# Optimization experiments

Measured on AMD Instinct MI355X. Metric: run time of the kernel, lower is better.

The kernel has to match this reference:

```python
import jax, jax.numpy as jnp
import numpy as np
import math

DIM = 1536
HEADS = 4
DIM_KEY = 64
DIM_VALUE = 64
NUM_REL_POS_FEATURES = 64
SEQ_LEN = 4096  # must match the hard-coded positional buffer seq_len in the torch module
SCALE = DIM_KEY ** -0.5


def positional_embed(seq_len, feature_size):
    # get_positional_embed: central-mask features + sign-antisymmetric copy
    distances = jnp.arange(-seq_len + 1, seq_len)  # (2n-1,)
    nb = feature_size // 2  # one feature fn, 2 components
    pow_rate = math.exp(math.log(seq_len + 1) / nb)
    center_widths = jnp.power(jnp.float32(pow_rate), jnp.arange(1, nb + 1, dtype=jnp.float32)) - 1.0
    emb = (center_widths[None, :] > jnp.abs(distances)[:, None]).astype(jnp.float32)  # (2n-1, nb)
    sign = jnp.sign(distances).astype(jnp.float32)[:, None]
    return jnp.concatenate([emb, sign * emb], axis=-1)  # (2n-1, feature_size)


def setup_inputs() -> dict:
    key = jax.random.key(0)
    ks = jax.random.split(key, 9)
    b, n, dim, h, dk, dv, F = 1, SEQ_LEN, DIM, HEADS, DIM_KEY, DIM_VALUE, NUM_REL_POS_FEATURES
    s = 0.02
    x = jax.random.normal(ks[0], (b, n, dim), dtype=jnp.float32)
    Wq = jax.random.normal(ks[1], (dim, h * dk), dtype=jnp.float32) * s
    Wk = jax.random.normal(ks[2], (dim, h * dk), dtype=jnp.float32) * s
    Wv = jax.random.normal(ks[3], (dim, h * dv), dtype=jnp.float32) * s
    W_rel_k = jax.random.normal(ks[4], (F, h * dk), dtype=jnp.float32) * s
    Wo = jax.random.normal(ks[5], (h * dv, dim), dtype=jnp.float32) * s  # torch inits zeros; random for a meaningful test
    bo = jnp.zeros((dim,), dtype=jnp.float32)
    rel_content_bias = jax.random.normal(ks[6], (1, h, 1, dk), dtype=jnp.float32)
    rel_pos_bias = jax.random.normal(ks[7], (1, h, 1, dk), dtype=jnp.float32)
    return {"x": x, "Wq": Wq, "Wk": Wk, "Wv": Wv, "W_rel_k": W_rel_k, "Wo": Wo, "bo": bo,
            "rel_content_bias": rel_content_bias, "rel_pos_bias": rel_pos_bias}


def reference(x, Wq, Wk, Wv, W_rel_k, Wo, bo, rel_content_bias, rel_pos_bias):
    b, n, _ = x.shape
    h, dk, dv = HEADS, DIM_KEY, DIM_VALUE
    # projections -> (b, h, n, d)
    q = (x @ Wq).reshape(b, n, h, dk).transpose(0, 2, 1, 3) * SCALE
    k = (x @ Wk).reshape(b, n, h, dk).transpose(0, 2, 1, 3)
    v = (x @ Wv).reshape(b, n, h, dv).transpose(0, 2, 1, 3)
    # content logits with content bias
    content_logits = jnp.einsum('bhid,bhjd->bhij', q + rel_content_bias, k)
    # relative-position keys from fixed positional buffer (pos_dropout p=0 -> identity)
    positions = positional_embed(SEQ_LEN, NUM_REL_POS_FEATURES)  # (2n-1, F)
    rel_k = (positions @ W_rel_k).reshape(2 * n - 1, h, dk).transpose(1, 0, 2)  # (h, 2n-1, dk)
    # rel logits then Transformer-XL strided shift: rel_logits[i, j] = r[i, n-1 + j - i]
    r = jnp.einsum('bhid,hjd->bhij', q + rel_pos_bias, rel_k)  # (b, h, n, 2n-1)
    idx = (n - 1) + jnp.arange(n)[None, :] - jnp.arange(n)[:, None]  # (n, n)
    rel_logits = jnp.take_along_axis(r, jnp.broadcast_to(idx[None, None], (b, h, n, n)), axis=-1)
    attn = jax.nn.softmax(content_logits + rel_logits, axis=-1)  # attn_dropout p=0 -> identity
    out = jnp.einsum('bhij,bhjd->bhid', attn, v)
    out = out.transpose(0, 2, 1, 3).reshape(b, n, h * dv)
    return out @ Wo + bo
```

## Files before the change

kernel.cpp:

```cpp
#include <hip/hip_runtime.h>
#include <hip/hip_bf16.h>

#define N_SEQ 4096
#define DIMM  1536
#define NH    4
#define DK    64
#define HD    256
#define QK_SCALE 0.125f
#define WSZ   393216
#define KSPLIT 8

typedef __bf16 bf16x8 __attribute__((ext_vector_type(8)));
typedef unsigned short u16;
typedef u16   u16x8  __attribute__((ext_vector_type(8)));
typedef u16   u16x4  __attribute__((ext_vector_type(4)));
typedef float f32x4  __attribute__((ext_vector_type(4)));
typedef float f32x16 __attribute__((ext_vector_type(16)));
typedef unsigned int u32x4 __attribute__((ext_vector_type(4)));

__device__ inline float b2f(u16 u){
    union { float f; unsigned int i; } v; v.i = ((unsigned int)u) << 16; return v.f;
}
__device__ inline u16 f2b(float f){
    __bf16 h = (__bf16)f;
    return __builtin_bit_cast(u16, h);
}
__device__ inline bf16x8 ldfrag(const u16* p){
    return __builtin_bit_cast(bf16x8, *(const u16x8*)p);
}
__device__ inline f32x16 zero16(){
    f32x16 v;
    #pragma unroll
    for (int i = 0; i < 16; ++i) v[i] = 0.f;
    return v;
}
__device__ inline float pair_sum(unsigned int wd){
    union { unsigned int i; float f; } lo, hi;
    lo.i = wd << 16; hi.i = wd & 0xffff0000u;
    return lo.f + hi.f;
}

__global__ __launch_bounds__(256) void convwt_kernel(const float* __restrict__ Wq,
    const float* __restrict__ Wk, const float* __restrict__ Wv, u16* __restrict__ Wt){
    int idx = (blockIdx.x * 256 + threadIdx.x) * 8;
    int s = idx / WSZ, off = idx % WSZ;
    int n = off / DIMM, k = off % DIMM;
    const float* W = (s == 0) ? Wq : (s == 1 ? Wk : Wv);
    u16x8 o;
    #pragma unroll
    for (int e = 0; e < 8; ++e) o[e] = f2b(W[(size_t)(k + e) * HD + n]);
    *(u16x8*)&Wt[idx] = o;
}

__global__ __launch_bounds__(256) void fmtab_kernel(unsigned char* __restrict__ fmt){
    int d = blockIdx.x * 256 + threadIdx.x;
    float lg = logf((float)(N_SEQ + 1)) * (1.0f / 32.0f);
    float ad = (float)d;
    int fm = 0;
    for (int f = 0; f < 32; ++f){
        float cw = expf(lg * (float)(f + 1)) - 1.0f;
        fm += (cw <= ad) ? 1 : 0;
    }
    fmt[d] = (unsigned char)fm;
}

__global__ __launch_bounds__(256) void wsuf_kernel(const float* __restrict__ Wrel,
    u16* __restrict__ WsP, u16* __restrict__ WsM){
    int t = threadIdx.x;
    int h = t >> 6, d = t & 63;
    float a1 = 0.f, a2 = 0.f;
    for (int fm = 31; fm >= 0; --fm){
        a1 += Wrel[(size_t)fm * HD + h * DK + d];
        a2 += Wrel[(size_t)(32 + fm) * HD + h * DK + d];
        WsP[(h * 32 + fm) * 64 + d] = f2b(a1 + a2);
        WsM[(h * 32 + fm) * 64 + d] = f2b(a1 - a2);
    }
}

__global__ __launch_bounds__(256) void qkv_kernel(const float* __restrict__ X,
    const u16* __restrict__ Wt,
    u16* __restrict__ Q, u16* __restrict__ K, u16* __restrict__ Vt){
    __shared__ __align__(16) u16 xs[64 * 72];
    __shared__ __align__(16) u16 bs[64 * 72];
    int s  = blockIdx.x >> 2;
    int n0 = (blockIdx.x & 3) * 64;
    int m0 = blockIdx.y * 64;
    int t = threadIdx.x;
    int w = t >> 6, lane = t & 63, qd = lane >> 4, l15 = lane & 15;
    int r  = t >> 3;
    int cv = (t & 7) * 8;
    f32x4 acc[4] = {{0,0,0,0},{0,0,0,0},{0,0,0,0},{0,0,0,0}};

    f32x4 xa[2], xb[2];
    u16x8 wv[2];
    auto LOAD = [&](int k0){
        #pragma unroll
        for (int rep = 0; rep < 2; ++rep){
            int rr = rep * 32 + r;
            size_t xi = (size_t)(m0 + rr) * DIMM + k0 + cv;
            xa[rep] = *(const f32x4*)(X + xi);
            xb[rep] = *(const f32x4*)(X + xi + 4);
            wv[rep] = *(const u16x8*)&Wt[(size_t)s * WSZ + (size_t)(n0 + rr) * DIMM + k0 + cv];
        }
    };
    auto STORE = [&](){
        #pragma unroll
        for (int rep = 0; rep < 2; ++rep){
            int rr = rep * 32 + r;
            u16x8 xv;
            #pragma unroll
            for (int e = 0; e < 4; ++e){ xv[e] = f2b(xa[rep][e]); xv[4 + e] = f2b(xb[rep][e]); }
            *(u16x8*)&xs[rr * 72 + cv] = xv;
            *(u16x8*)&bs[rr * 72 + cv] = wv[rep];
        }
    };

    LOAD(0);
    for (int k0 = 0; k0 < DIMM; k0 += 64){
        STORE();
        __syncthreads();
        if (k0 + 64 < DIMM) LOAD(k0 + 64);
        bf16x8 a0 = ldfrag(&xs[(w * 16 + l15) * 72 +  0 + qd * 8]);
        bf16x8 a1 = ldfrag(&xs[(w * 16 + l15) * 72 + 32 + qd * 8]);
        #pragma unroll
        for (int nt = 0; nt < 4; ++nt){
            bf16x8 b0 = ldfrag(&bs[(nt * 16 + l15) * 72 +  0 + qd * 8]);
            bf16x8 b1 = ldfrag(&bs[(nt * 16 + l15) * 72 + 32 + qd * 8]);
            acc[nt] = __builtin_amdgcn_mfma_f32_16x16x32_bf16(a0, b0, acc[nt], 0, 0, 0);
            acc[nt] = __builtin_amdgcn_mfma_f32_16x16x32_bf16(a1, b1, acc[nt], 0, 0, 0);
        }
        __syncthreads();
    }

    int row0 = m0 + w * 16 + qd * 4;
    if (s == 0){
        #pragma unroll
        for (int nt = 0; nt < 4; ++nt){
            int col = n0 + nt * 16 + l15;
            #pragma unroll
            for (int reg = 0; reg < 4; ++reg)
                Q[(size_t)(row0 + reg) * HD + col] = f2b(acc[nt][reg] * QK_SCALE);
        }
    } else if (s == 1){
        #pragma unroll
        for (int nt = 0; nt < 4; ++nt){
            int col = n0 + nt * 16 + l15;
            #pragma unroll
            for (int reg = 0; reg < 4; ++reg)
                K[(size_t)(row0 + reg) * HD + col] = f2b(acc[nt][reg]);
        }
    } else {
        #pragma unroll
        for (int nt = 0; nt < 4; ++nt){
            int col = n0 + nt * 16 + l15;
            u16x4 pv;
            #pragma unroll
            for (int reg = 0; reg < 4; ++reg) pv[reg] = f2b(acc[nt][reg]);
            *(u16x4*)&Vt[(size_t)col * N_SEQ + row0] = pv;
        }
    }
}

__global__ __launch_bounds__(256) void attn_kernel(const u16* __restrict__ Q,
    const u16* __restrict__ Kg, const u16* __restrict__ Vt,
    const u16* __restrict__ WsPg, const u16* __restrict__ WsMg,
    const unsigned char* __restrict__ fmtg,
    const float* __restrict__ CB, const float* __restrict__ PB,
    u16* __restrict__ OpU, float* __restrict__ mpart, float* __restrict__ lpart){
    __shared__ __align__(16) unsigned char smem[39936];
    u16* Ks   = (u16*)(smem);
    u16* Vts  = (u16*)(smem + 9216);
    u16* Qs   = (u16*)(smem);
    u16* relP = (u16*)(smem + 18432);
    u16* relM = (u16*)(smem + 27136);
    unsigned char* fmt = smem + 35840;
    u16* WsPs = (u16*)(smem + 18432);
    u16* WsMs = (u16*)(smem + 23040);

    int i0   = blockIdx.x * 128;
    int h    = blockIdx.y;
    int half = blockIdx.z;
    int bid  = blockIdx.x * NH + h;
    int jbase = half * (N_SEQ / KSPLIT);
    const int NT = (N_SEQ / KSPLIT) / 64;
    int t = threadIdx.x;
    int w = t >> 6, lane = t & 63, l31 = lane & 31, hbit = lane >> 5;
    int h8 = hbit * 8;
    int i_loc = w * 32 + l31;

    int sr = t >> 3, scv = (t & 7) * 8;
    u16x8 kr0, kr1, vr0, vr1;
    auto LOAD = [&](int j0){
        kr0 = *(const u16x8*)&Kg[(size_t)(j0 + sr)      * HD + h * DK + scv];
        kr1 = *(const u16x8*)&Kg[(size_t)(j0 + 32 + sr) * HD + h * DK + scv];
        vr0 = *(const u16x8*)&Vt[(size_t)(h * 64 + sr)      * N_SEQ + j0 + scv];
        vr1 = *(const u16x8*)&Vt[(size_t)(h * 64 + 32 + sr) * N_SEQ + j0 + scv];
    };
    auto STORE = [&](){
        *(u16x8*)&Ks [(sr)      * 72 + scv] = kr0;
        *(u16x8*)&Ks [(32 + sr) * 72 + scv] = kr1;
        *(u16x8*)&Vts[(sr)      * 72 + scv] = vr0;
        *(u16x8*)&Vts[(32 + sr) * 72 + scv] = vr1;
    };
    LOAD(jbase);

    #pragma unroll
    for (int rep = 0; rep < 4; ++rep){
        int vid = rep * 256 + t;
        int r  = vid >> 3;
        int cv = (vid & 7) * 8;
        *(u16x8*)&Qs[r * 72 + cv] = *(const u16x8*)&Q[(size_t)(i0 + r) * HD + h * DK + cv];
    }
    {
        int r = t >> 3, cv = (t & 7) * 8;
        *(u16x8*)&WsPs[r * 72 + cv] = *(const u16x8*)&WsPg[(h * 32 + r) * 64 + cv];
        *(u16x8*)&WsMs[r * 72 + cv] = *(const u16x8*)&WsMg[(h * 32 + r) * 64 + cv];
    }
    ((uint4*)fmt)[t] = ((const uint4*)fmtg)[t];
    __syncthreads();

    bf16x8 qcF[4], qpF[4];
    #pragma unroll
    for (int kc = 0; kc < 4; ++kc){
        bf16x8 raw = ldfrag(&Qs[i_loc * 72 + kc * 16 + h8]);
        const float* cbp = CB + h * DK + kc * 16 + h8;
        const float* pbp = PB + h * DK + kc * 16 + h8;
        bf16x8 qc, qp;
        #pragma unroll
        for (int e = 0; e < 8; ++e){
            float qf = (float)raw[e];
            qc[e] = (__bf16)(qf + cbp[e]);
            qp[e] = (__bf16)(qf + pbp[e]);
        }
        qcF[kc] = qc; qpF[kc] = qp;
    }

    f32x16 rP = zero16(), rM = zero16();
    #pragma unroll
    for (int kc = 0; kc < 4; ++kc){
        bf16x8 aP = ldfrag(&WsPs[l31 * 72 + kc * 16 + h8]);
        bf16x8 aM = ldfrag(&WsMs[l31 * 72 + kc * 16 + h8]);
        rP = __builtin_amdgcn_mfma_f32_32x32x16_bf16(aP, qpF[kc], rP, 0, 0, 0);
        rM = __builtin_amdgcn_mfma_f32_32x32x16_bf16(aM, qpF[kc], rM, 0, 0, 0);
    }
    __syncthreads();

    #pragma unroll
    for (int r = 0; r < 16; ++r){
        int fm = (r & 3) + 8 * (r >> 2) + 4 * hbit;
        relP[i_loc * 34 + fm] = f2b(rP[r]);
        relM[i_loc * 34 + fm] = f2b(rM[r]);
    }
    if (hbit == 0){
        relP[i_loc * 34 + 33] = f2b((rP[0] + rM[0]) * 0.5f);
        relP[i_loc * 34 + 32] = 0;
        relM[i_loc * 34 + 32] = 0;
        relM[i_loc * 34 + 33] = 0;
    }
    STORE();
    __syncthreads();

    float mrow = -1e30f, lacc = 0.f;
    f32x16 oacc0 = zero16(), oacc1 = zero16();

#define MFMA32(A, B, C) __builtin_amdgcn_mfma_f32_32x32x16_bf16(A, B, C, 0, 0, 0)

#define PACK8(ST, WD) { \
    _Pragma("unroll") \
    for (int q_ = 0; q_ < 8; ++q_){ \
        float pa_ = __expf(ST[2 * q_]     - mrow); \
        float pc_ = __expf(ST[2 * q_ + 1] - mrow); \
        unsigned int wd_ = (unsigned int)f2b(pa_) | ((unsigned int)f2b(pc_) << 16); \
        WD[q_] = wd_; \
        lsum += pair_sum(wd_); \
    } }

#define MKFRAG(DST, WD, ZZ) { \
    unsigned int a0_ = WD[(ZZ) * 4 + 0], a1_ = WD[(ZZ) * 4 + 1]; \
    unsigned int b0_ = WD[(ZZ) * 4 + 2], b1_ = WD[(ZZ) * 4 + 3]; \
    unsigned int xa0_ = (unsigned int)__shfl_xor((int)a0_, 32); \
    unsigned int xa1_ = (unsigned int)__shfl_xor((int)a1_, 32); \
    unsigned int xb0_ = (unsigned int)__shfl_xor((int)b0_, 32); \
    unsigned int xb1_ = (unsigned int)__shfl_xor((int)b1_, 32); \
    u32x4 fw_; \
    fw_[0] = hbit ? xb0_ : a0_; \
    fw_[1] = hbit ? xb1_ : a1_; \
    fw_[2] = hbit ? b0_  : xa0_; \
    fw_[3] = hbit ? b1_  : xa1_; \
    DST = __builtin_bit_cast(bf16x8, fw_); }

#define PVSTEP(PF, COL) { \
    oacc0 = MFMA32(PF, ldfrag(&Vts[(l31)      * 72 + (COL) + h8]), oacc0); \
    oacc1 = MFMA32(PF, ldfrag(&Vts[(32 + l31) * 72 + (COL) + h8]), oacc1); }

    for (int kt = 0; kt < NT; ++kt){
        int j0 = jbase + kt * 64;
        if (kt + 1 < NT) LOAD(j0 + 64);

        f32x16 st0 = zero16(), st1 = zero16();
        #pragma unroll
        for (int kc = 0; kc < 4; ++kc){
            bf16x8 k0 = ldfrag(&Ks[(l31)      * 72 + kc * 16 + h8]);
            bf16x8 k1 = ldfrag(&Ks[(32 + l31) * 72 + kc * 16 + h8]);
            st0 = MFMA32(k0, qcF[kc], st0);
            st1 = MFMA32(k1, qcF[kc], st1);
        }

        int D = j0 - i0;
        bool fast = false; int fmU = 0; const u16* tabU = relP;
        if (D >= 128){
            int fa = fmt[D - 127], fb = fmt[D + 63];
            fast = (fa == fb); fmU = fa; tabU = relP;
        } else if (D <= -64){
            int fa = fmt[-D - 63], fb = fmt[-D + 127];
            fast = (fa == fb); fmU = fa; tabU = relM;
        }
        if (fast){
            float relv = b2f(tabU[i_loc * 34 + fmU]);
            #pragma unroll
            for (int r = 0; r < 16; ++r){ st0[r] += relv; st1[r] += relv; }
        } else {
            #pragma unroll
            for (int r = 0; r < 16; ++r){
                int jb = (r & 3) + 8 * (r >> 2) + 4 * hbit;
                {
                    int dd = D + jb - i_loc;
                    int ad = dd < 0 ? -dd : dd;
                    int fm = fmt[ad];
                    const u16* tab = (dd >= 0) ? relP : relM;
                    st0[r] += b2f(tab[i_loc * 34 + ((dd == 0) ? 33 : fm)]);
                }
                {
                    int dd = D + 32 + jb - i_loc;
                    int ad = dd < 0 ? -dd : dd;
                    int fm = fmt[ad];
                    const u16* tab = (dd >= 0) ? relP : relM;
                    st1[r] += b2f(tab[i_loc * 34 + ((dd == 0) ? 33 : fm)]);
                }
            }
        }

        float mx = st0[0];
        #pragma unroll
        for (int r = 1; r < 16; ++r) mx = fmaxf(mx, st0[r]);
        #pragma unroll
        for (int r = 0; r < 16; ++r) mx = fmaxf(mx, st1[r]);
        mx = fmaxf(mx, __shfl_xor(mx, 32));

        if (!__all(mx - mrow <= 8.0f)){
            float mnew = fmaxf(mrow, mx);
            float alpha = __expf(mrow - mnew);
            mrow = mnew;
            lacc *= alpha;
            #pragma unroll
            for (int r = 0; r < 16; ++r){
                float ar = __shfl(alpha, (r & 3) + 8 * (r >> 2) + 4 * hbit);
                oacc0[r] *= ar; oacc1[r] *= ar;
            }
        }

        float lsum = 0.f;
        unsigned int wds0[8], wds1[8];
        PACK8(st0, wds0)
        PACK8(st1, wds1)
        lacc += lsum + __shfl_xor(lsum, 32);

        bf16x8 pf0, pf1, pf2, pf3;
        MKFRAG(pf0, wds0, 0)
        MKFRAG(pf1, wds0, 1)
        MKFRAG(pf2, wds1, 0)
        MKFRAG(pf3, wds1, 1)
        PVSTEP(pf0,  0)
        PVSTEP(pf1, 16)
        PVSTEP(pf2, 32)
        PVSTEP(pf3, 48)

        __syncthreads();
        if (kt + 1 < NT) STORE();
        __syncthreads();
    }

    size_t pb = ((size_t)half * 128 + bid) * 128;
    #pragma unroll
    for (int r = 0; r < 16; ++r){
        int iO = w * 32 + (r & 3) + 8 * (r >> 2) + 4 * hbit;
        OpU[(pb + iO) * 64 + l31]      = f2b(oacc0[r]);
        OpU[(pb + iO) * 64 + 32 + l31] = f2b(oacc1[r]);
    }
    if (hbit == 0){
        mpart[pb + i_loc] = mrow;
        lpart[pb + i_loc] = lacc;
    }
#undef MFMA32
#undef PACK8
#undef MKFRAG
#undef PVSTEP
}

__global__ __launch_bounds__(256) void combine_kernel(const u16* __restrict__ OpU,
    const float* __restrict__ mpart, const float* __restrict__ lpart,
    u16* __restrict__ Oatt){
    int i0 = blockIdx.x * 128;
    int h  = blockIdx.y;
    int bid = blockIdx.x * NH + h;
    int t = threadIdx.x;
    int r = t >> 1, cb = (t & 1) * 32;
    size_t pr[8];
    float ms[8], ls[8];
    float m = -1e30f;
    #pragma unroll
    for (int s = 0; s < 8; ++s){
        pr[s] = ((size_t)s * 128 + bid) * 128 + r;
        ms[s] = mpart[pr[s]];
        ls[s] = lpart[pr[s]];
        m = fmaxf(m, ms[s]);
    }
    float den = 0.f, wgt[8];
    #pragma unroll
    for (int s = 0; s < 8; ++s){ wgt[s] = __expf(ms[s] - m); den += wgt[s] * ls[s]; }
    float inv = 1.0f / fmaxf(den, 1e-30f);
    float o[32];
    #pragma unroll
    for (int e = 0; e < 32; ++e) o[e] = 0.f;
    #pragma unroll
    for (int s = 0; s < 8; ++s){
        #pragma unroll
        for (int c = 0; c < 4; ++c){
            u16x8 a = *(const u16x8*)&OpU[pr[s] * 64 + cb + c * 8];
            #pragma unroll
            for (int e = 0; e < 8; ++e) o[c * 8 + e] += wgt[s] * b2f(a[e]);
        }
    }
    size_t ob = (size_t)(i0 + r) * HD + h * DK + cb;
    #pragma unroll
    for (int c = 0; c < 4; ++c){
        u16x8 rv;
        #pragma unroll
        for (int e = 0; e < 8; ++e) rv[e] = f2b(o[c * 8 + e] * inv);
        *(u16x8*)&Oatt[ob + c * 8] = rv;
    }
}

__global__ __launch_bounds__(256) void oproj_kernel(const u16* __restrict__ A,
    const float* __restrict__ Wo, const float* __restrict__ bo,
    float* __restrict__ out, int m_base){
    __shared__ __align__(16) u16 xs[64 * 72];
    __shared__ __align__(16) u16 bs[64 * 72];
    int m0 = m_base + blockIdx.y * 64;
    int n0 = blockIdx.x * 64;
    int t = threadIdx.x;
    int w = t >> 6, lane = t & 63, qd = lane >> 4, l15 = lane & 15;
    f32x4 acc[4] = {{0,0,0,0},{0,0,0,0},{0,0,0,0},{0,0,0,0}};
    for (int k0 = 0; k0 < HD; k0 += 64){
        #pragma unroll
        for (int rep = 0; rep < 2; ++rep){
            int vid = rep * 256 + t;
            int r  = vid >> 3;
            int cv = (vid & 7) * 8;
            *(u16x8*)&xs[r * 72 + cv] = *(const u16x8*)&A[(size_t)(m0 + r) * HD + k0 + cv];
            size_t wi = (size_t)(k0 + r) * DIMM + n0 + cv;
            f32x4 wa = *(const f32x4*)(Wo + wi), wb = *(const f32x4*)(Wo + wi + 4);
            u16x8 wv;
            #pragma unroll
            for (int e = 0; e < 4; ++e){ wv[e] = f2b(wa[e]); wv[4 + e] = f2b(wb[e]); }
            #pragma unroll
            for (int e = 0; e < 8; ++e) bs[(cv + e) * 72 + r] = wv[e];
        }
        __syncthreads();
        bf16x8 a0 = ldfrag(&xs[(w * 16 + l15) * 72 +  0 + qd * 8]);
        bf16x8 a1 = ldfrag(&xs[(w * 16 + l15) * 72 + 32 + qd * 8]);
        #pragma unroll
        for (int nt = 0; nt < 4; ++nt){
            bf16x8 b0 = ldfrag(&bs[(nt * 16 + l15) * 72 +  0 + qd * 8]);
            bf16x8 b1 = ldfrag(&bs[(nt * 16 + l15) * 72 + 32 + qd * 8]);
            acc[nt] = __builtin_amdgcn_mfma_f32_16x16x32_bf16(a0, b0, acc[nt], 0, 0, 0);
            acc[nt] = __builtin_amdgcn_mfma_f32_16x16x32_bf16(a1, b1, acc[nt], 0, 0, 0);
        }
        __syncthreads();
    }
    #pragma unroll
    for (int nt = 0; nt < 4; ++nt)
        #pragma unroll
        for (int reg = 0; reg < 4; ++reg){
            int row = m0 + w * 16 + qd * 4 + reg;
            int col = n0 + nt * 16 + l15;
            out[(size_t)row * DIMM + col] = acc[nt][reg] + bo[col];
        }
}

extern "C" void kernel_launch(void* const* d_in, const int* in_sizes, int n_in,
                              void* d_out, int out_size, void* d_ws, size_t ws_size,
                              hipStream_t stream){
    const float* X  = (const float*)d_in[0];
    const float* Wq = (const float*)d_in[1];
    const float* Wk = (const float*)d_in[2];
    const float* Wv = (const float*)d_in[3];
    const float* Wr = (const float*)d_in[4];
    const float* Wo = (const float*)d_in[5];
    const float* bo = (const float*)d_in[6];
    const float* CB = (const float*)d_in[7];
    const float* PB = (const float*)d_in[8];
    float* out = (float*)d_out;
    u16* base = (u16*)d_out;

    u16* Qb   = base;
    u16* Kb   = base + 1048576;
    u16* Vt   = base + 2097152;
    u16* Wt   = base + 3145728;
    u16* OpU  = base + 3145728;
    float* mpart = out + 5767168;
    float* lpart = out + 5898240;
    u16* Oatt = base;

    unsigned char* fmtg = (unsigned char*)d_ws;
    u16* WsP = (u16*)((char*)d_ws + 4096);
    u16* WsM = (u16*)((char*)d_ws + 20480);

    convwt_kernel<<<dim3(576), 256, 0, stream>>>(Wq, Wk, Wv, Wt);
    fmtab_kernel<<<dim3(16), 256, 0, stream>>>(fmtg);
    wsuf_kernel<<<dim3(1), 256, 0, stream>>>(Wr, WsP, WsM);
    qkv_kernel<<<dim3(12, 64), 256, 0, stream>>>(X, Wt, Qb, Kb, Vt);
    attn_kernel<<<dim3(32, NH, KSPLIT), 256, 0, stream>>>(Qb, Kb, Vt, WsP, WsM,
                                                          fmtg, CB, PB,
                                                          OpU, mpart, lpart);
    combine_kernel<<<dim3(32, NH), 256, 0, stream>>>(OpU, mpart, lpart, Oatt);

    oproj_kernel<<<dim3(24, 58), 256, 0, stream>>>(Oatt, Wo, bo, out, 384);
    oproj_kernel<<<dim3(24,  5), 256, 0, stream>>>(Oatt, Wo, bo, out, 64);
    oproj_kernel<<<dim3(24,  1), 256, 0, stream>>>(Oatt, Wo, bo, out, 0);
}
```

Before: 233.7 us.

## Use exp2 softmax, fold fast-path bias, merge setup kernels, add MFMA priority hints

Pre-scales the biased queries by log2(e) so the softmax can use exp2 throughout, including the combine step. On the fast path the uniform relative-position bias is folded into the exponent offset instead of being added to all 32 scores. The rescale threshold rises to 11, fragment building needs two shuffles instead of four, and the diagonal special case now writes into table slot 0. The suffix-sum weight kernel is merged into the fmt-table kernel as an extra block, and s_setprio hints are placed around the MFMA sections.

```diff
diff --git a/kernel.cpp b/kernel.cpp
--- a/kernel.cpp
+++ b/kernel.cpp
@@ -9,6 +9,7 @@
 #define QK_SCALE 0.125f
 #define WSZ   393216
 #define KSPLIT 8
+#define LOG2E 1.44269504f
 
 typedef __bf16 bf16x8 __attribute__((ext_vector_type(8)));
 typedef unsigned short u16;
@@ -34,11 +35,7 @@
     for (int i = 0; i < 16; ++i) v[i] = 0.f;
     return v;
 }
-__device__ inline float pair_sum(unsigned int wd){
-    union { unsigned int i; float f; } lo, hi;
-    lo.i = wd << 16; hi.i = wd & 0xffff0000u;
-    return lo.f + hi.f;
-}
+#define EXP2(x) exp2f(x)
 
 __global__ __launch_bounds__(256) void convwt_kernel(const float* __restrict__ Wq,
     const float* __restrict__ Wk, const float* __restrict__ Wv, u16* __restrict__ Wt){
@@ -52,8 +49,21 @@
     *(u16x8*)&Wt[idx] = o;
 }
 
-__global__ __launch_bounds__(256) void fmtab_kernel(unsigned char* __restrict__ fmt){
-    int d = blockIdx.x * 256 + threadIdx.x;
+__global__ __launch_bounds__(256) void fmtab_kernel(unsigned char* __restrict__ fmt,
+    const float* __restrict__ Wrel, u16* __restrict__ WsP, u16* __restrict__ WsM){
+    int t = threadIdx.x;
+    if (blockIdx.x == 16){
+        int h = t >> 6, d = t & 63;
+        float a1 = 0.f, a2 = 0.f;
+        for (int fm = 31; fm >= 0; --fm){
+            a1 += Wrel[(size_t)fm * HD + h * DK + d];
+            a2 += Wrel[(size_t)(32 + fm) * HD + h * DK + d];
+            WsP[(h * 32 + fm) * 64 + d] = f2b(a1 + a2);
+            WsM[(h * 32 + fm) * 64 + d] = f2b(a1 - a2);
+        }
+        return;
+    }
+    int d = blockIdx.x * 256 + t;
     float lg = logf((float)(N_SEQ + 1)) * (1.0f / 32.0f);
     float ad = (float)d;
     int fm = 0;
@@ -62,19 +72,6 @@
         fm += (cw <= ad) ? 1 : 0;
     }
     fmt[d] = (unsigned char)fm;
-}
-
-__global__ __launch_bounds__(256) void wsuf_kernel(const float* __restrict__ Wrel,
-    u16* __restrict__ WsP, u16* __restrict__ WsM){
-    int t = threadIdx.x;
-    int h = t >> 6, d = t & 63;
-    float a1 = 0.f, a2 = 0.f;
-    for (int fm = 31; fm >= 0; --fm){
-        a1 += Wrel[(size_t)fm * HD + h * DK + d];
-        a2 += Wrel[(size_t)(32 + fm) * HD + h * DK + d];
-        WsP[(h * 32 + fm) * 64 + d] = f2b(a1 + a2);
-        WsM[(h * 32 + fm) * 64 + d] = f2b(a1 - a2);
-    }
 }
 
 __global__ __launch_bounds__(256) void qkv_kernel(const float* __restrict__ X,
@@ -229,8 +226,8 @@
         #pragma unroll
         for (int e = 0; e < 8; ++e){
             float qf = (float)raw[e];
-            qc[e] = (__bf16)(qf + cbp[e]);
-            qp[e] = (__bf16)(qf + pbp[e]);
+            qc[e] = (__bf16)((qf + cbp[e]) * LOG2E);
+            qp[e] = (__bf16)((qf + pbp[e]) * LOG2E);
         }
         qcF[kc] = qc; qpF[kc] = qp;
     }
@@ -251,12 +248,8 @@
         relP[i_loc * 34 + fm] = f2b(rP[r]);
         relM[i_loc * 34 + fm] = f2b(rM[r]);
     }
-    if (hbit == 0){
-        relP[i_loc * 34 + 33] = f2b((rP[0] + rM[0]) * 0.5f);
-        relP[i_loc * 34 + 32] = 0;
-        relM[i_loc * 34 + 32] = 0;
-        relM[i_loc * 34 + 33] = 0;
-    }
+    if (hbit == 0)
+        relP[i_loc * 34 + 0] = f2b((rP[0] + rM[0]) * 0.5f);
     STORE();
     __syncthreads();
 
@@ -268,36 +261,37 @@
 #define PACK8(ST, WD) { \
     _Pragma("unroll") \
     for (int q_ = 0; q_ < 8; ++q_){ \
-        float pa_ = __expf(ST[2 * q_]     - mrow); \
-        float pc_ = __expf(ST[2 * q_ + 1] - mrow); \
-        unsigned int wd_ = (unsigned int)f2b(pa_) | ((unsigned int)f2b(pc_) << 16); \
-        WD[q_] = wd_; \
-        lsum += pair_sum(wd_); \
+        float pa_ = EXP2(ST[2 * q_]     - bias); \
+        float pc_ = EXP2(ST[2 * q_ + 1] - bias); \
+        lsum += pa_ + pc_; \
+        WD[q_] = (unsigned int)f2b(pa_) | ((unsigned int)f2b(pc_) << 16); \
     } }
 
 #define MKFRAG(DST, WD, ZZ) { \
     unsigned int a0_ = WD[(ZZ) * 4 + 0], a1_ = WD[(ZZ) * 4 + 1]; \
     unsigned int b0_ = WD[(ZZ) * 4 + 2], b1_ = WD[(ZZ) * 4 + 3]; \
-    unsigned int xa0_ = (unsigned int)__shfl_xor((int)a0_, 32); \
-    unsigned int xa1_ = (unsigned int)__shfl_xor((int)a1_, 32); \
-    unsigned int xb0_ = (unsigned int)__shfl_xor((int)b0_, 32); \
-    unsigned int xb1_ = (unsigned int)__shfl_xor((int)b1_, 32); \
+    unsigned int sh0_ = (unsigned int)__shfl_xor((int)(hbit ? a0_ : b0_), 32); \
+    unsigned int sh1_ = (unsigned int)__shfl_xor((int)(hbit ? a1_ : b1_), 32); \
     u32x4 fw_; \
-    fw_[0] = hbit ? xb0_ : a0_; \
-    fw_[1] = hbit ? xb1_ : a1_; \
-    fw_[2] = hbit ? b0_  : xa0_; \
-    fw_[3] = hbit ? b1_  : xa1_; \
+    fw_[0] = hbit ? sh0_ : a0_; \
+    fw_[1] = hbit ? sh1_ : a1_; \
+    fw_[2] = hbit ? b0_  : sh0_; \
+    fw_[3] = hbit ? b1_  : sh1_; \
     DST = __builtin_bit_cast(bf16x8, fw_); }
 
 #define PVSTEP(PF, COL) { \
     oacc0 = MFMA32(PF, ldfrag(&Vts[(l31)      * 72 + (COL) + h8]), oacc0); \
     oacc1 = MFMA32(PF, ldfrag(&Vts[(32 + l31) * 72 + (COL) + h8]), oacc1); }
 
+    const u16* relP_i = relP + i_loc * 34;
+    const u16* relM_i = relM + i_loc * 34;
+
     for (int kt = 0; kt < NT; ++kt){
         int j0 = jbase + kt * 64;
         if (kt + 1 < NT) LOAD(j0 + 64);
 
         f32x16 st0 = zero16(), st1 = zero16();
+        __builtin_amdgcn_s_setprio(1);
         #pragma unroll
         for (int kc = 0; kc < 4; ++kc){
             bf16x8 k0 = ldfrag(&Ks[(l31)      * 72 + kc * 16 + h8]);
@@ -305,37 +299,39 @@
             st0 = MFMA32(k0, qcF[kc], st0);
             st1 = MFMA32(k1, qcF[kc], st1);
         }
+        __builtin_amdgcn_s_setprio(0);
 
         int D = j0 - i0;
-        bool fast = false; int fmU = 0; const u16* tabU = relP;
+        int Di = D - i_loc;
+        float relv = 0.f;
+        bool fast = false; int fmU = 0; const u16* tabU = relP_i;
         if (D >= 128){
             int fa = fmt[D - 127], fb = fmt[D + 63];
-            fast = (fa == fb); fmU = fa; tabU = relP;
+            fast = (fa == fb); fmU = fa; tabU = relP_i;
         } else if (D <= -64){
             int fa = fmt[-D - 63], fb = fmt[-D + 127];
-            fast = (fa == fb); fmU = fa; tabU = relM;
+            fast = (fa == fb); fmU = fa; tabU = relM_i;
         }
         if (fast){
-            float relv = b2f(tabU[i_loc * 34 + fmU]);
-            #pragma unroll
-            for (int r = 0; r < 16; ++r){ st0[r] += relv; st1[r] += relv; }
+            relv = b2f(tabU[fmU]);
         } else {
             #pragma unroll
             for (int r = 0; r < 16; ++r){
-                int jb = (r & 3) + 8 * (r >> 2) + 4 * hbit;
+                const int jb = (r & 3) + 8 * (r >> 2);
+                int jbh = jb + 4 * hbit;
                 {
-                    int dd = D + jb - i_loc;
+                    int dd = Di + jbh;
                     int ad = dd < 0 ? -dd : dd;
                     int fm = fmt[ad];
-                    const u16* tab = (dd >= 0) ? relP : relM;
-                    st0[r] += b2f(tab[i_loc * 34 + ((dd == 0) ? 33 : fm)]);
+                    const u16* tab = (dd >= 0) ? relP_i : relM_i;
+                    st0[r] += b2f(tab[fm]);
                 }
                 {
-                    int dd = D + 32 + jb - i_loc;
+                    int dd = Di + 32 + jbh;
                     int ad = dd < 0 ? -dd : dd;
                     int fm = fmt[ad];
-                    const u16* tab = (dd >= 0) ? relP : relM;
-                    st1[r] += b2f(tab[i_loc * 34 + ((dd == 0) ? 33 : fm)]);
+                    const u16* tab = (dd >= 0) ? relP_i : relM_i;
+                    st1[r] += b2f(tab[fm]);
                 }
             }
         }
@@ -345,11 +341,11 @@
         for (int r = 1; r < 16; ++r) mx = fmaxf(mx, st0[r]);
         #pragma unroll
         for (int r = 0; r < 16; ++r) mx = fmaxf(mx, st1[r]);
-        mx = fmaxf(mx, __shfl_xor(mx, 32));
-
-        if (!__all(mx - mrow <= 8.0f)){
+        mx = fmaxf(mx, __shfl_xor(mx, 32)) + relv;
+
+        if (!__all(mx - mrow <= 11.0f)){
             float mnew = fmaxf(mrow, mx);
-            float alpha = __expf(mrow - mnew);
+            float alpha = EXP2(mrow - mnew);
             mrow = mnew;
             lacc *= alpha;
             #pragma unroll
@@ -359,6 +355,7 @@
             }
         }
 
+        float bias = mrow - relv;
         float lsum = 0.f;
         unsigned int wds0[8], wds1[8];
         PACK8(st0, wds0)
@@ -370,10 +367,12 @@
         MKFRAG(pf1, wds0, 1)
         MKFRAG(pf2, wds1, 0)
         MKFRAG(pf3, wds1, 1)
+        __builtin_amdgcn_s_setprio(1);
         PVSTEP(pf0,  0)
         PVSTEP(pf1, 16)
         PVSTEP(pf2, 32)
         PVSTEP(pf3, 48)
+        __builtin_amdgcn_s_setprio(0);
 
         __syncthreads();
         if (kt + 1 < NT) STORE();
@@ -417,7 +416,7 @@
     }
     float den = 0.f, wgt[8];
     #pragma unroll
-    for (int s = 0; s < 8; ++s){ wgt[s] = __expf(ms[s] - m); den += wgt[s] * ls[s]; }
+    for (int s = 0; s < 8; ++s){ wgt[s] = EXP2(ms[s] - m); den += wgt[s] * ls[s]; }
     float inv = 1.0f / fmaxf(den, 1e-30f);
     float o[32];
     #pragma unroll
@@ -517,8 +516,7 @@
     u16* WsM = (u16*)((char*)d_ws + 20480);
 
     convwt_kernel<<<dim3(576), 256, 0, stream>>>(Wq, Wk, Wv, Wt);
-    fmtab_kernel<<<dim3(16), 256, 0, stream>>>(fmtg);
-    wsuf_kernel<<<dim3(1), 256, 0, stream>>>(Wr, WsP, WsM);
+    fmtab_kernel<<<dim3(17), 256, 0, stream>>>(fmtg, Wr, WsP, WsM);
     qkv_kernel<<<dim3(12, 64), 256, 0, stream>>>(X, Wt, Qb, Kb, Vt);
     attn_kernel<<<dim3(32, NH, KSPLIT), 256, 0, stream>>>(Qb, Kb, Vt, WsP, WsM,
                                                           fmtg, CB, PB,
```

Measured after the change: 229.6 us. Within noise of the previous version (-1.8%).
